# Kernel tuning notes

Measured on AMD Instinct MI355X. Metric: run time of the kernel, lower is better.

## Reference

```python
import jax, jax.numpy as jnp
import numpy as np

N_NODES = 50000
N_EDGES = 800000
D_IN, D_HID, D_OUT = 128, 256, 128


def setup_inputs() -> dict:
    key = jax.random.key(0)
    ks = jax.random.split(key, 8)
    x = jax.random.normal(ks[0], (N_NODES, D_IN), dtype=jnp.float32)
    edge_src = jax.random.randint(ks[1], (N_EDGES,), 0, N_NODES, dtype=jnp.int32)
    edge_dst = jnp.sort(jax.random.randint(ks[2], (N_EDGES,), 0, N_NODES, dtype=jnp.int32))
    edge_val = jax.random.uniform(ks[3], (N_EDGES,), dtype=jnp.float32)
    eps = jnp.zeros((1,), dtype=jnp.float32)
    w1 = jax.random.normal(ks[4], (D_IN, D_HID), dtype=jnp.float32) * (1.0 / np.sqrt(D_IN))
    b1 = jnp.zeros((D_HID,), dtype=jnp.float32)
    w2 = jax.random.normal(ks[5], (D_HID, D_OUT), dtype=jnp.float32) * (1.0 / np.sqrt(D_HID))
    b2 = jnp.zeros((D_OUT,), dtype=jnp.float32)
    return {"x": x, "edge_src": edge_src, "edge_dst": edge_dst, "edge_val": edge_val,
            "eps": eps, "w1": w1, "b1": b1, "w2": w2, "b2": b2}


def reference(x, edge_src, edge_dst, edge_val, eps, w1, b1, w2, b2):
    # Sparse adjacency aggregation: (A @ x)[i] = sum_{e: dst=i} val_e * x[src_e]
    msgs = edge_val[:, None] * x[edge_src]            # [E, D_IN]
    agg = jax.ops.segment_sum(msgs, edge_dst, num_segments=N_NODES)  # [N, D_IN]
    h = agg + (1.0 + eps[0]) * x                      # AX + (1+eps)X
    # 2-layer MLP
    h = jax.nn.relu(h @ w1 + b1)                      # [N, D_HID]
    out = h @ w2 + b2                                 # [N, D_OUT]
    return out
```

## Files before the change

### kernel.cpp

```cpp
#include <hip/hip_runtime.h>
#include <hip/hip_bf16.h>
#include <cstdint>

#define N_NODES 50000
#define N_EDGES 800000
#define D_IN 128
#define D_HID 256
#define D_OUT 128

typedef __bf16 bf16;
typedef __bf16 bf16x8 __attribute__((ext_vector_type(8)));
typedef __bf16 bf16x4 __attribute__((ext_vector_type(4)));
typedef float f32x4 __attribute__((ext_vector_type(4)));

__global__ __launch_bounds__(256) void prep_kernel(
    const float* __restrict__ x,
    const float* __restrict__ w1, const float* __restrict__ w2,
    bf16* __restrict__ xb, bf16* __restrict__ w1t, bf16* __restrict__ w2t) {
  const int i = blockIdx.x * 256 + threadIdx.x;
  float4 v = ((const float4*)x)[i];
  ((bf16x4*)xb)[i] = bf16x4{(bf16)v.x, (bf16)v.y, (bf16)v.z, (bf16)v.w};
  if (i < D_IN * D_HID) {
    int k = i >> 8, n = i & 255;
    w1t[n * D_IN + k] = (bf16)w1[i];
  } else if (i < 2 * D_IN * D_HID) {
    int j = i - D_IN * D_HID;
    int k = j >> 7, n = j & 127;
    w2t[n * D_HID + k] = (bf16)w2[j];
  }
}

__global__ __launch_bounds__(256) void csr_kernel(
    const int* __restrict__ dst, int* __restrict__ offs) {
  const int e = blockIdx.x * 256 + threadIdx.x;
  if (e >= N_EDGES) return;
  const int b = dst[e];
  const int a = (e == 0) ? -1 : dst[e - 1];
  for (int n = a + 1; n <= b; ++n) offs[n] = e;
  if (e == N_EDGES - 1)
    for (int n = b + 1; n <= N_NODES; ++n) offs[n] = N_EDGES;
}

__global__ __launch_bounds__(256) void node_agg_kernel(
    const bf16* __restrict__ xb, const int* __restrict__ src,
    const float* __restrict__ val, const int* __restrict__ offs,
    const float* __restrict__ eps, bf16* __restrict__ aggb) {
  const int node = __builtin_amdgcn_readfirstlane(
      (blockIdx.x << 2) | (threadIdx.x >> 6));
  const int lane = threadIdx.x & 63;
  const int s = __builtin_amdgcn_readfirstlane(offs[node]);
  const int e = __builtin_amdgcn_readfirstlane(offs[node + 1]);

  float2 acc = make_float2(0.f, 0.f);
  int i = s;
  for (; i + 8 <= e; i += 8) {
    int sv[8]; float vv[8]; int g[8];
    #pragma unroll
    for (int t = 0; t < 8; ++t) { sv[t] = src[i + t]; vv[t] = val[i + t]; }
    #pragma unroll
    for (int t = 0; t < 8; ++t)
      g[t] = *(const int*)&xb[(long)sv[t] * D_IN + lane * 2];
    #pragma unroll
    for (int t = 0; t < 8; ++t) {
      float gx = __uint_as_float((unsigned)g[t] << 16);
      float gy = __uint_as_float((unsigned)g[t] & 0xffff0000u);
      acc.x = fmaf(vv[t], gx, acc.x);
      acc.y = fmaf(vv[t], gy, acc.y);
    }
  }
  for (; i < e; ++i) {
    int sv = src[i]; float vv = val[i];
    int g = *(const int*)&xb[(long)sv * D_IN + lane * 2];
    acc.x = fmaf(vv, __uint_as_float((unsigned)g << 16), acc.x);
    acc.y = fmaf(vv, __uint_as_float((unsigned)g & 0xffff0000u), acc.y);
  }

  const float scale = 1.0f + eps[0];
  int xg = *(const int*)&xb[(long)node * D_IN + lane * 2];
  acc.x = fmaf(scale, __uint_as_float((unsigned)xg << 16), acc.x);
  acc.y = fmaf(scale, __uint_as_float((unsigned)xg & 0xffff0000u), acc.y);

  union { struct { bf16 x, y; } h; int i_; } u;
  u.h.x = (bf16)acc.x; u.h.y = (bf16)acc.y;
  *(int*)&aggb[(long)node * D_IN + lane * 2] = u.i_;
}

__global__ __launch_bounds__(256) void mlp_fused(
    const bf16* __restrict__ A, const bf16* __restrict__ W1t,
    const bf16* __restrict__ W2t, const float* __restrict__ b1,
    const float* __restrict__ b2, float* __restrict__ out) {
  constexpr int LDA = 136;
  constexpr int LDH = 264;
  __shared__ alignas(16) bf16 As[64][LDA];
  __shared__ alignas(16) bf16 Hs[64][LDH];

  const int tid = threadIdx.x;
  const int m0 = blockIdx.x * 64;
  const int wave = tid >> 6;
  const int lane = tid & 63;
  const int l15 = lane & 15;
  const int quad = lane >> 4;

  #pragma unroll
  for (int it = 0; it < 4; ++it) {
    int idx = tid + it * 256;
    int r = idx >> 4;
    int c8 = (idx & 15) << 3;
    int row = m0 + r; if (row >= N_NODES) row = N_NODES - 1;
    *(bf16x8*)&As[r][c8] = *(const bf16x8*)&A[(long)row * D_IN + c8];
  }

  bf16x8 w1f[4][4];
  #pragma unroll
  for (int nf = 0; nf < 4; ++nf) {
    int n = wave * 64 + nf * 16 + l15;
    #pragma unroll
    for (int ks = 0; ks < 4; ++ks)
      w1f[nf][ks] = *(const bf16x8*)&W1t[(long)n * D_IN + ks * 32 + quad * 8];
  }
  __syncthreads();

  f32x4 acc[4][4] = {};
  #pragma unroll
  for (int ks = 0; ks < 4; ++ks) {
    int kq = ks * 32 + quad * 8;
    bf16x8 a[4];
    #pragma unroll
    for (int mf = 0; mf < 4; ++mf)
      a[mf] = *(const bf16x8*)&As[mf * 16 + l15][kq];
    #pragma unroll
    for (int mf = 0; mf < 4; ++mf)
      #pragma unroll
      for (int nf = 0; nf < 4; ++nf)
        acc[mf][nf] = __builtin_amdgcn_mfma_f32_16x16x32_bf16(
            a[mf], w1f[nf][ks], acc[mf][nf], 0, 0, 0);
  }

  #pragma unroll
  for (int nf = 0; nf < 4; ++nf) {
    int col = wave * 64 + nf * 16 + l15;
    float bv = b1[col];
    #pragma unroll
    for (int mf = 0; mf < 4; ++mf)
      #pragma unroll
      for (int r = 0; r < 4; ++r)
        Hs[mf * 16 + quad * 4 + r][col] = (bf16)fmaxf(acc[mf][nf][r] + bv, 0.f);
  }

  bf16x8 w2f[2][8];
  #pragma unroll
  for (int nf2 = 0; nf2 < 2; ++nf2) {
    int n = wave * 32 + nf2 * 16 + l15;
    #pragma unroll
    for (int ks2 = 0; ks2 < 8; ++ks2)
      w2f[nf2][ks2] = *(const bf16x8*)&W2t[(long)n * D_HID + ks2 * 32 + quad * 8];
  }
  __syncthreads();

  f32x4 acc2[4][2] = {};
  #pragma unroll
  for (int ks2 = 0; ks2 < 8; ++ks2) {
    int kq = ks2 * 32 + quad * 8;
    bf16x8 ha[4];
    #pragma unroll
    for (int mf = 0; mf < 4; ++mf)
      ha[mf] = *(const bf16x8*)&Hs[mf * 16 + l15][kq];
    #pragma unroll
    for (int mf = 0; mf < 4; ++mf)
      #pragma unroll
      for (int nf2 = 0; nf2 < 2; ++nf2)
        acc2[mf][nf2] = __builtin_amdgcn_mfma_f32_16x16x32_bf16(
            ha[mf], w2f[nf2][ks2], acc2[mf][nf2], 0, 0, 0);
  }

  #pragma unroll
  for (int nf2 = 0; nf2 < 2; ++nf2) {
    int col = wave * 32 + nf2 * 16 + l15;
    float bv = b2[col];
    #pragma unroll
    for (int mf = 0; mf < 4; ++mf)
      #pragma unroll
      for (int r = 0; r < 4; ++r) {
        int row = m0 + mf * 16 + quad * 4 + r;
        if (row < N_NODES)
          out[(long)row * D_OUT + col] = acc2[mf][nf2][r] + bv;
      }
  }
}

extern "C" void kernel_launch(void* const* d_in, const int* in_sizes, int n_in,
                              void* d_out, int out_size, void* d_ws, size_t ws_size,
                              hipStream_t stream) {
  const float* x    = (const float*)d_in[0];
  const int*   esrc = (const int*)d_in[1];
  const int*   edst = (const int*)d_in[2];
  const float* evl  = (const float*)d_in[3];
  const float* eps  = (const float*)d_in[4];
  const float* w1   = (const float*)d_in[5];
  const float* b1   = (const float*)d_in[6];
  const float* w2   = (const float*)d_in[7];
  const float* b2   = (const float*)d_in[8];
  float* out = (float*)d_out;

  bf16* aggb = (bf16*)d_ws;
  bf16* xb   = aggb + (size_t)N_NODES * D_IN;
  bf16* w1t  = xb + (size_t)N_NODES * D_IN;
  bf16* w2t  = w1t + D_IN * D_HID;
  int*  offs = (int*)(w2t + D_HID * D_OUT);

  prep_kernel<<<(N_NODES * D_IN / 4) / 256, 256, 0, stream>>>(
      x, w1, w2, xb, w1t, w2t);
  csr_kernel<<<(N_EDGES + 255) / 256, 256, 0, stream>>>(edst, offs);
  node_agg_kernel<<<(N_NODES + 3) / 4, 256, 0, stream>>>(
      xb, esrc, evl, offs, eps, aggb);
  mlp_fused<<<(N_NODES + 63) / 64, 256, 0, stream>>>(
      aggb, w1t, w2t, b1, b2, out);
}
```

Baseline: 156.1 us.

## Window source gathers by node range, fuse CSR build into prep, nontemporal stores

The CSR offset build is folded into the prep kernel, saving one launch. The aggregation kernel now walks each node's edge list once per source-node window (8192 nodes each), and only gathers the rows that fall in the current window. The aim is to keep each window's slice of the bf16 feature table resident in cache. This costs re-reading src and val about seven times and running more masked loop iterations per node. Output and aggregate stores become nontemporal to avoid polluting the cache.

```diff
diff --git a/kernel.cpp b/kernel.cpp
--- a/kernel.cpp
+++ b/kernel.cpp
@@ -8,15 +8,19 @@
 #define D_HID 256
 #define D_OUT 128
 
+#define WIN_SHIFT 13
+#define N_WIN ((N_NODES + (1 << WIN_SHIFT) - 1) >> WIN_SHIFT)
+
 typedef __bf16 bf16;
 typedef __bf16 bf16x8 __attribute__((ext_vector_type(8)));
 typedef __bf16 bf16x4 __attribute__((ext_vector_type(4)));
 typedef float f32x4 __attribute__((ext_vector_type(4)));
 
-__global__ __launch_bounds__(256) void prep_kernel(
-    const float* __restrict__ x,
+__global__ __launch_bounds__(256) void prep_csr_kernel(
+    const float* __restrict__ x, const int* __restrict__ dst,
     const float* __restrict__ w1, const float* __restrict__ w2,
-    bf16* __restrict__ xb, bf16* __restrict__ w1t, bf16* __restrict__ w2t) {
+    bf16* __restrict__ xb, bf16* __restrict__ w1t, bf16* __restrict__ w2t,
+    int* __restrict__ offs) {
   const int i = blockIdx.x * 256 + threadIdx.x;
   float4 v = ((const float4*)x)[i];
   ((bf16x4*)xb)[i] = bf16x4{(bf16)v.x, (bf16)v.y, (bf16)v.z, (bf16)v.w};
@@ -28,17 +32,13 @@
     int k = j >> 7, n = j & 127;
     w2t[n * D_HID + k] = (bf16)w2[j];
   }
-}
-
-__global__ __launch_bounds__(256) void csr_kernel(
-    const int* __restrict__ dst, int* __restrict__ offs) {
-  const int e = blockIdx.x * 256 + threadIdx.x;
-  if (e >= N_EDGES) return;
-  const int b = dst[e];
-  const int a = (e == 0) ? -1 : dst[e - 1];
-  for (int n = a + 1; n <= b; ++n) offs[n] = e;
-  if (e == N_EDGES - 1)
-    for (int n = b + 1; n <= N_NODES; ++n) offs[n] = N_EDGES;
+  if (i < N_EDGES) {
+    const int b = dst[i];
+    const int a = (i == 0) ? -1 : dst[i - 1];
+    for (int n = a + 1; n <= b; ++n) offs[n] = i;
+    if (i == N_EDGES - 1)
+      for (int n = b + 1; n <= N_NODES; ++n) offs[n] = N_EDGES;
+  }
 }
 
 __global__ __launch_bounds__(256) void node_agg_kernel(
@@ -52,27 +52,35 @@
   const int e = __builtin_amdgcn_readfirstlane(offs[node + 1]);
 
   float2 acc = make_float2(0.f, 0.f);
-  int i = s;
-  for (; i + 8 <= e; i += 8) {
-    int sv[8]; float vv[8]; int g[8];
-    #pragma unroll
-    for (int t = 0; t < 8; ++t) { sv[t] = src[i + t]; vv[t] = val[i + t]; }
-    #pragma unroll
-    for (int t = 0; t < 8; ++t)
-      g[t] = *(const int*)&xb[(long)sv[t] * D_IN + lane * 2];
-    #pragma unroll
-    for (int t = 0; t < 8; ++t) {
-      float gx = __uint_as_float((unsigned)g[t] << 16);
-      float gy = __uint_as_float((unsigned)g[t] & 0xffff0000u);
-      acc.x = fmaf(vv[t], gx, acc.x);
-      acc.y = fmaf(vv[t], gy, acc.y);
+
+  if (e > s) {
+    for (int w = 0; w < N_WIN; ++w) {
+      for (int i = s; i < e; i += 16) {
+        int sv[16]; float vv[16];
+        #pragma unroll
+        for (int t = 0; t < 16; ++t) {
+          int idx = i + t; if (idx >= e) idx = e - 1;
+          sv[t] = src[idx];
+          vv[t] = val[idx];
+        }
+        int g[16];
+        #pragma unroll
+        for (int t = 0; t < 16; ++t) {
+          if ((i + t < e) && ((sv[t] >> WIN_SHIFT) == w)) {
+            g[t] = *(const int*)&xb[(long)sv[t] * D_IN + lane * 2];
+          } else {
+            g[t] = 0; vv[t] = 0.f;
+          }
+        }
+        #pragma unroll
+        for (int t = 0; t < 16; ++t) {
+          float gx = __uint_as_float((unsigned)g[t] << 16);
+          float gy = __uint_as_float((unsigned)g[t] & 0xffff0000u);
+          acc.x = fmaf(vv[t], gx, acc.x);
+          acc.y = fmaf(vv[t], gy, acc.y);
+        }
+      }
     }
-  }
-  for (; i < e; ++i) {
-    int sv = src[i]; float vv = val[i];
-    int g = *(const int*)&xb[(long)sv * D_IN + lane * 2];
-    acc.x = fmaf(vv, __uint_as_float((unsigned)g << 16), acc.x);
-    acc.y = fmaf(vv, __uint_as_float((unsigned)g & 0xffff0000u), acc.y);
   }
 
   const float scale = 1.0f + eps[0];
@@ -82,7 +90,7 @@
 
   union { struct { bf16 x, y; } h; int i_; } u;
   u.h.x = (bf16)acc.x; u.h.y = (bf16)acc.y;
-  *(int*)&aggb[(long)node * D_IN + lane * 2] = u.i_;
+  __builtin_nontemporal_store(u.i_, (int*)&aggb[(long)node * D_IN + lane * 2]);
 }
 
 __global__ __launch_bounds__(256) void mlp_fused(
@@ -183,7 +191,8 @@
       for (int r = 0; r < 4; ++r) {
         int row = m0 + mf * 16 + quad * 4 + r;
         if (row < N_NODES)
-          out[(long)row * D_OUT + col] = acc2[mf][nf2][r] + bv;
+          __builtin_nontemporal_store(acc2[mf][nf2][r] + bv,
+                                      &out[(long)row * D_OUT + col]);
       }
   }
 }
@@ -208,9 +217,8 @@
   bf16* w2t  = w1t + D_IN * D_HID;
   int*  offs = (int*)(w2t + D_HID * D_OUT);
 
-  prep_kernel<<<(N_NODES * D_IN / 4) / 256, 256, 0, stream>>>(
-      x, w1, w2, xb, w1t, w2t);
-  csr_kernel<<<(N_EDGES + 255) / 256, 256, 0, stream>>>(edst, offs);
+  prep_csr_kernel<<<(N_NODES * D_IN / 4) / 256, 256, 0, stream>>>(
+      x, edst, w1, w2, xb, w1t, w2t, offs);
   node_agg_kernel<<<(N_NODES + 3) / 4, 256, 0, stream>>>(
       xb, esrc, evl, offs, eps, aggb);
   mlp_fused<<<(N_NODES + 63) / 64, 256, 0, stream>>>(
```

Result: slower. 558.5 us (+257.7%).
